# Optimization experiments

Hardware: AMD Instinct MI355X
Metric: run time of the kernel (lower is better)

The kernel has to match this reference:

```python
import jax, jax.numpy as jnp
import numpy as np

L, D_IN, D_HID, D_OUT, N = 8, 256, 1024, 256, 32768


def setup_inputs() -> dict:
    key = jax.random.key(0)
    kx, kp, kw1, kw2 = jax.random.split(key, 4)
    x = jax.random.normal(kx, (N, D_IN), dtype=jnp.float32)
    plane_idx = jax.random.randint(kp, (N,), 0, L, dtype=jnp.int32)
    W1 = jax.random.normal(kw1, (L, D_HID, D_IN), dtype=jnp.float32) * 0.014
    b1 = jnp.zeros((L, D_HID), dtype=jnp.float32)
    W2 = jax.random.normal(kw2, (L, D_OUT, D_HID), dtype=jnp.float32) * np.float32((2.0 / D_HID) ** 0.5)
    b2 = jnp.zeros((L, D_OUT), dtype=jnp.float32)
    return {"x": x, "W1": W1, "b1": b1, "W2": W2, "b2": b2, "plane_idx": plane_idx}


def reference(x, W1, b1, W2, b2, plane_idx):
    # Dense-dispatch MoE reference: scan over the L planes, run the full
    # 2-layer MLP for each plane's weights, and select per-walker rows via
    # the plane mask (equivalent math to gather -> MLP -> scatter).
    n_planes = W1.shape[0]
    out0 = jnp.zeros((x.shape[0], W2.shape[1]), dtype=x.dtype)

    def plane_step(out, p):
        h = jax.nn.gelu(x @ W1[p].T + b1[p], approximate=False)  # [N, D_hid]
        o = h @ W2[p].T + b2[p]                                  # [N, D_out]
        out = jnp.where((plane_idx == p)[:, None], o, out)
        return out, None

    out, _ = jax.lax.scan(plane_step, out0, jnp.arange(n_planes))
    return out
```

## Files before the change

kernel.cpp:

```cpp
#include <hip/hip_runtime.h>
#include <hip/hip_fp16.h>
#include <cstdint>

#define NT      32768
#define DIN     256
#define DHID    1024
#define DOUT    256
#define NPLANES 8
#define NBLK    (NT / 256)

typedef unsigned short u16;
typedef __attribute__((ext_vector_type(8))) _Float16 f16x8;
typedef __attribute__((ext_vector_type(4))) float    f32x4;

#define WS_OFFSETS 0
#define WS_META    64
#define WS_TP      1024
#define WS_TM      (WS_TP + 544*4)
#define WS_BLKHIST (WS_TM + 544*4)
#define WS_BLKBASE (WS_BLKHIST + NBLK*8*4)
#define WS_PERM    (WS_BLKBASE + NBLK*8*4)
#define WS_XB      (WS_PERM + NT*4)
#define WS_W1B     (WS_XB + NT*DIN*2)
#define WS_W2B     (WS_W1B + NPLANES*DHID*DIN*2)
#define WS_HB      (WS_W2B + NPLANES*DOUT*DHID*2)

__device__ __forceinline__ u16 f2h_bits(float f) {
    __half h = __float2half(f);
    return *reinterpret_cast<u16*>(&h);
}

__device__ __forceinline__ void gl_lds16(const void* g, void* l) {
    __builtin_amdgcn_global_load_lds(
        (const __attribute__((address_space(1))) void*)g,
        (__attribute__((address_space(3))) void*)l,
        16, 0, 0);
}

__device__ __forceinline__ float gelu_fast(float x) {
    const float u = x * (1.5957691216f + 0.07135481283f * x * x);
    const float e = __expf(-u);
    return x * __builtin_amdgcn_rcpf(1.0f + e);
}

__global__ void prep_k(const int* __restrict__ pidx, const float* __restrict__ x,
                       const float* __restrict__ W1, const float* __restrict__ W2,
                       int* __restrict__ blkhist, u16* __restrict__ xb,
                       u16* __restrict__ w1b, u16* __restrict__ w2b) {
    __shared__ int cnt[NPLANES];
    const int t = threadIdx.x, lane = t & 63;
    if ((int)blockIdx.x < NBLK) {
        if (t < NPLANES) cnt[t] = 0;
        __syncthreads();
        const int p = pidx[blockIdx.x * 256 + t];
#pragma unroll
        for (int q = 0; q < NPLANES; ++q) {
            unsigned long long m = __ballot(p == q);
            if (p == q && __popcll(m & ((1ULL << lane) - 1)) == 0)
                atomicAdd(&cnt[q], __popcll(m));
        }
        __syncthreads();
        if (t < NPLANES) blkhist[blockIdx.x * NPLANES + t] = cnt[t];
    }
    const int n0 = NT * DIN / 4, n1 = NPLANES * DHID * DIN / 4, n2 = NPLANES * DOUT * DHID / 4;
    const int stride = gridDim.x * blockDim.x;
    for (int i = blockIdx.x * blockDim.x + t; i < n0 + n1 + n2; i += stride) {
        const float4* s; ushort4* d; int j;
        if (i < n0)           { s = (const float4*)x;  d = (ushort4*)xb;  j = i; }
        else if (i < n0 + n1) { s = (const float4*)W1; d = (ushort4*)w1b; j = i - n0; }
        else                  { s = (const float4*)W2; d = (ushort4*)w2b; j = i - n0 - n1; }
        float4 v = s[j];
        ushort4 o;
        o.x = f2h_bits(v.x); o.y = f2h_bits(v.y);
        o.z = f2h_bits(v.z); o.w = f2h_bits(v.w);
        d[j] = o;
    }
}

__global__ void scan_k(const int* __restrict__ blkhist, int* __restrict__ offsets,
                       int* __restrict__ blkbase, int* __restrict__ meta,
                       int* __restrict__ tp, int* __restrict__ tm) {
    __shared__ int tot[NPLANES];
    const int t = threadIdx.x;
    if (t < NPLANES) {
        int s = 0;
#pragma unroll 8
        for (int b = 0; b < NBLK; ++b) s += blkhist[b * NPLANES + t];
        tot[t] = s;
    }
    __syncthreads();
    if (t == 0) {
        int off = 0, tc = 0;
        for (int p = 0; p < NPLANES; ++p) {
            offsets[p] = off;
            for (int m = 0; m < tot[p]; m += 64) { tp[tc] = p; tm[tc] = m; ++tc; }
            off += tot[p];
        }
        offsets[NPLANES] = off;
        meta[0] = tc;
    }
    __syncthreads();
    if (t < NPLANES) {
        int run = offsets[t];
#pragma unroll 8
        for (int b = 0; b < NBLK; ++b) {
            blkbase[b * NPLANES + t] = run;
            run += blkhist[b * NPLANES + t];
        }
    }
}

__global__ void scatter_k(const int* __restrict__ pidx, const int* __restrict__ blkbase,
                          int* __restrict__ perm) {
    __shared__ int wcnt[4][NPLANES];
    __shared__ int wbase[4][NPLANES];
    const int t = threadIdx.x, lane = t & 63, wave = t >> 6;
    const int i = blockIdx.x * 256 + t;
    const int p = pidx[i];
    int rank = 0;
#pragma unroll
    for (int q = 0; q < NPLANES; ++q) {
        unsigned long long m = __ballot(p == q);
        if (lane == 0) wcnt[wave][q] = __popcll(m);
        if (p == q) rank = __popcll(m & ((1ULL << lane) - 1));
    }
    __syncthreads();
    if (t < NPLANES) {
        int run = blkbase[blockIdx.x * NPLANES + t];
#pragma unroll
        for (int w = 0; w < 4; ++w) { wbase[w][t] = run; run += wcnt[w][t]; }
    }
    __syncthreads();
    perm[wbase[wave][p] + rank] = i;
}

#define XCD_MAP(NSPLIT)                                                        \
    const int ntiles = meta[0];                                                \
    const int xcd = blockIdx.x & 7, idx = blockIdx.x >> 3;                     \
    const int q8 = ntiles >> 3, r8 = ntiles & 7;                               \
    const int tn = q8 + (xcd < r8 ? 1 : 0);                                    \
    if (idx >= tn * (NSPLIT)) return;                                          \
    const int tile = (xcd < r8 ? xcd * (q8 + 1)                                \
                               : r8 * (q8 + 1) + (xcd - r8) * q8)              \
                     + idx / (NSPLIT);                                         \
    const int n0v = (idx % (NSPLIT)) * 128;

__global__ __launch_bounds__(256, 6) void gemm1_k(
    const u16* __restrict__ xb, const u16* __restrict__ w1b,
    const float* __restrict__ b1, const int* __restrict__ perm,
    const int* __restrict__ offsets, const int* __restrict__ meta,
    const int* __restrict__ tp, const int* __restrict__ tm,
    u16* __restrict__ hb)
{
    __shared__ __align__(16) u16 smem[12288];
    XCD_MAP(8)
    const int p   = tp[tile];
    const int m0  = tm[tile];
    const int off = offsets[p];
    const int cnt = offsets[p + 1] - off;

    u16* const sA = smem;
    u16* const sB = smem + 4096;

    const int tid = threadIdx.x;
    const u16* aptr[2];
    const u16* bptr[4];
#pragma unroll
    for (int c = 0; c < 2; ++c) {
        const int slot = c * 256 + tid, row = slot >> 3, ch = slot & 7;
        const int gr = min(m0 + row, cnt - 1);
        aptr[c] = xb + (size_t)perm[off + gr] * DIN + ((ch ^ (row & 7)) * 8);
    }
#pragma unroll
    for (int c = 0; c < 4; ++c) {
        const int slot = c * 256 + tid, row = slot >> 3, ch = slot & 7;
        bptr[c] = w1b + ((size_t)p * DHID + n0v + row) * DIN + ((ch ^ (row & 7)) * 8);
    }
    const int wave = tid >> 6, lane = tid & 63;
    const int wr = wave >> 1, wc = wave & 1;
    const int lm = lane & 15, lk = lane >> 4;

    f32x4 acc[2][4];
#pragma unroll
    for (int a = 0; a < 2; ++a)
#pragma unroll
        for (int b = 0; b < 4; ++b) acc[a][b] = (f32x4){0.f, 0.f, 0.f, 0.f};

    for (int kt = 0; kt < DIN / 64; ++kt) {
        const int k0 = kt * 64;
#pragma unroll
        for (int c = 0; c < 2; ++c) gl_lds16(aptr[c] + k0, sA + c * 2048 + tid * 8);
#pragma unroll
        for (int c = 0; c < 4; ++c) gl_lds16(bptr[c] + k0, sB + c * 2048 + tid * 8);
        __syncthreads();
#pragma unroll
        for (int kk = 0; kk < 2; ++kk) {
            f16x8 af[2], bf[4];
#pragma unroll
            for (int mf = 0; mf < 2; ++mf) {
                const int row = wr * 32 + mf * 16 + lm;
                const int g   = kk * 4 + lk;
                af[mf] = *(const f16x8*)(sA + row * 64 + ((g ^ (row & 7)) * 8));
            }
#pragma unroll
            for (int nf = 0; nf < 4; ++nf) {
                const int row = wc * 64 + nf * 16 + lm;
                const int g   = kk * 4 + lk;
                bf[nf] = *(const f16x8*)(sB + row * 64 + ((g ^ (row & 7)) * 8));
            }
#pragma unroll
            for (int mf = 0; mf < 2; ++mf)
#pragma unroll
                for (int nf = 0; nf < 4; ++nf)
                    acc[mf][nf] = __builtin_amdgcn_mfma_f32_16x16x32_f16(
                        af[mf], bf[nf], acc[mf][nf], 0, 0, 0);
        }
        __syncthreads();
    }

    u16* const sOut = smem;
#pragma unroll
    for (int nf = 0; nf < 4; ++nf) {
        const int col = wc * 64 + nf * 16 + lm;
        const float bb = b1[p * DHID + n0v + col];
        const int cc = col >> 3, c7 = col & 7;
#pragma unroll
        for (int mf = 0; mf < 2; ++mf) {
#pragma unroll
            for (int j = 0; j < 4; ++j) {
                const int tok = wr * 32 + mf * 16 + lk * 4 + j;
                sOut[tok * 128 + ((cc ^ (tok & 15)) * 8) + c7] =
                    f2h_bits(gelu_fast(acc[mf][nf][j] + bb));
            }
        }
    }
    __syncthreads();
    const int r = tid >> 2, qq = tid & 3;
    if (m0 + r < cnt) {
        u16* dst = hb + (size_t)(off + m0 + r) * DHID + n0v;
#pragma unroll
        for (int c = 0; c < 4; ++c) {
            const int l = qq * 4 + c;
            *(int4*)(dst + l * 8) = *(const int4*)(sOut + r * 128 + ((l ^ (r & 15)) * 8));
        }
    }
}

__global__ __launch_bounds__(256, 3) void gemm2_k(
    const u16* __restrict__ hb, const u16* __restrict__ w2b,
    const float* __restrict__ b2, const int* __restrict__ perm,
    const int* __restrict__ offsets, const int* __restrict__ meta,
    const int* __restrict__ tp, const int* __restrict__ tm,
    float* __restrict__ out)
{
    __shared__ __align__(16) u16 smem[24576];
    XCD_MAP(2)
    const int p   = tp[tile];
    const int m0  = tm[tile];
    const int off = offsets[p];
    const int cnt = offsets[p + 1] - off;

    u16* const sA = smem;
    u16* const sB = smem + 8192;

    const int tid = threadIdx.x;
    const u16* aptr[4];
#pragma unroll
    for (int c = 0; c < 4; ++c) {
        const int slot = c * 256 + tid, row = slot >> 4, ch = slot & 15;
        aptr[c] = hb + (size_t)(off + min(m0 + row, cnt - 1)) * DHID + ((ch ^ (row & 15)) * 8);
    }
    const u16* bptr[8];
#pragma unroll
    for (int c = 0; c < 8; ++c) {
        const int slot = c * 256 + tid, row = slot >> 4, ch = slot & 15;
        bptr[c] = w2b + ((size_t)p * DOUT + n0v + row) * DHID + ((ch ^ (row & 15)) * 8);
    }
    const int wave = tid >> 6, lane = tid & 63;
    const int wr = wave >> 1, wc = wave & 1;
    const int lm = lane & 15, lk = lane >> 4;

    f32x4 acc[2][4];
#pragma unroll
    for (int a = 0; a < 2; ++a)
#pragma unroll
        for (int b = 0; b < 4; ++b) acc[a][b] = (f32x4){0.f, 0.f, 0.f, 0.f};

    for (int kt = 0; kt < DHID / 128; ++kt) {
        const int k0 = kt * 128;
#pragma unroll
        for (int c = 0; c < 4; ++c) gl_lds16(aptr[c] + k0, sA + c * 2048 + tid * 8);
#pragma unroll
        for (int c = 0; c < 8; ++c) gl_lds16(bptr[c] + k0, sB + c * 2048 + tid * 8);
        __syncthreads();
#pragma unroll
        for (int kk = 0; kk < 4; ++kk) {
            f16x8 af[2], bf[4];
#pragma unroll
            for (int mf = 0; mf < 2; ++mf) {
                const int row = wr * 32 + mf * 16 + lm;
                const int g   = kk * 4 + lk;
                af[mf] = *(const f16x8*)(sA + row * 128 + ((g ^ (row & 15)) * 8));
            }
#pragma unroll
            for (int nf = 0; nf < 4; ++nf) {
                const int row = wc * 64 + nf * 16 + lm;
                const int g   = kk * 4 + lk;
                bf[nf] = *(const f16x8*)(sB + row * 128 + ((g ^ (row & 15)) * 8));
            }
#pragma unroll
            for (int mf = 0; mf < 2; ++mf)
#pragma unroll
                for (int nf = 0; nf < 4; ++nf)
                    acc[mf][nf] = __builtin_amdgcn_mfma_f32_16x16x32_f16(
                        af[mf], bf[nf], acc[mf][nf], 0, 0, 0);
        }
        __syncthreads();
    }

#pragma unroll
    for (int nf = 0; nf < 4; ++nf) {
        const int col = n0v + wc * 64 + nf * 16 + lm;
        const float bb = b2[p * DOUT + col];
#pragma unroll
        for (int mf = 0; mf < 2; ++mf) {
#pragma unroll
            for (int j = 0; j < 4; ++j) {
                const int tok = wr * 32 + mf * 16 + lk * 4 + j;
                if (m0 + tok < cnt)
                    out[(size_t)perm[off + m0 + tok] * DOUT + col] = acc[mf][nf][j] + bb;
            }
        }
    }
}

extern "C" void kernel_launch(void* const* d_in, const int* in_sizes, int n_in,
                              void* d_out, int out_size, void* d_ws, size_t ws_size,
                              hipStream_t stream) {
    const float* x    = (const float*)d_in[0];
    const float* W1   = (const float*)d_in[1];
    const float* b1   = (const float*)d_in[2];
    const float* W2   = (const float*)d_in[3];
    const float* b2   = (const float*)d_in[4];
    const int*   pidx = (const int*)d_in[5];
    float*       out  = (float*)d_out;

    char* ws      = (char*)d_ws;
    int* offsets  = (int*)(ws + WS_OFFSETS);
    int* meta     = (int*)(ws + WS_META);
    int* tp       = (int*)(ws + WS_TP);
    int* tm       = (int*)(ws + WS_TM);
    int* blkhist  = (int*)(ws + WS_BLKHIST);
    int* blkbase  = (int*)(ws + WS_BLKBASE);
    int* perm     = (int*)(ws + WS_PERM);
    u16* xb       = (u16*)(ws + WS_XB);
    u16* w1b      = (u16*)(ws + WS_W1B);
    u16* w2b      = (u16*)(ws + WS_W2B);
    u16* hb       = (u16*)(ws + WS_HB);

    prep_k<<<2048, 256, 0, stream>>>(pidx, x, W1, W2, blkhist, xb, w1b, w2b);
    scan_k<<<1, 64, 0, stream>>>(blkhist, offsets, blkbase, meta, tp, tm);
    scatter_k<<<NBLK, 256, 0, stream>>>(pidx, blkbase, perm);

    gemm1_k<<<4224, 256, 0, stream>>>(xb, w1b, b1, perm, offsets, meta, tp, tm, hb);
    gemm2_k<<<1056, 256, 0, stream>>>(hb, w2b, b2, perm, offsets, meta, tp, tm, out);
}
```

Measured before the change: 114.7 us.

## Unify GEMM kernels with double-buffered LDS weights and direct-to-register A loads

```diff
diff --git a/kernel.cpp b/kernel.cpp
--- a/kernel.cpp
+++ b/kernel.cpp
@@ -145,190 +145,149 @@
                      + idx / (NSPLIT);                                         \
     const int n0v = (idx % (NSPLIT)) * 128;
 
-__global__ __launch_bounds__(256, 6) void gemm1_k(
-    const u16* __restrict__ xb, const u16* __restrict__ w1b,
-    const float* __restrict__ b1, const int* __restrict__ perm,
+#define LOADA(dst, KTX)                                                        \
+    {                                                                          \
+        _Pragma("unroll") for (int mf = 0; mf < 2; ++mf) {                     \
+            const u16* ar = mf ? arow1 : arow0;                                \
+            _Pragma("unroll") for (int ks = 0; ks < 2; ++ks)                   \
+                dst[mf][ks] = *(const f16x8*)(ar + (KTX) * 64 + ks * 32);      \
+        }                                                                      \
+    }
+#define STAGEW(buf, KTX)                                                       \
+    {                                                                          \
+        _Pragma("unroll") for (int c = 0; c < 4; ++c)                          \
+            gl_lds16(wsrc[c] + (KTX) * 64, (buf) + c * 2048 + tid * 8);        \
+    }
+#define COMPUTE(buf, a)                                                        \
+    {                                                                          \
+        _Pragma("unroll") for (int kk = 0; kk < 2; ++kk) {                     \
+            f16x8 bf[4];                                                       \
+            _Pragma("unroll") for (int nf = 0; nf < 4; ++nf) {                 \
+                const int row = wc * 64 + nf * 16 + lm;                        \
+                bf[nf] = *(const f16x8*)((buf) + row * 64 +                    \
+                                         (((kk * 4 + lk) ^ (row & 7)) * 8));   \
+            }                                                                  \
+            _Pragma("unroll") for (int mf = 0; mf < 2; ++mf)                   \
+                _Pragma("unroll") for (int nf = 0; nf < 4; ++nf)               \
+                    acc[mf][nf] = __builtin_amdgcn_mfma_f32_16x16x32_f16(      \
+                        a[mf][kk], bf[nf], acc[mf][nf], 0, 0, 0);              \
+        }                                                                      \
+    }
+
+template<bool L1>
+__global__ __launch_bounds__(256, 4) void gemm_k(
+    const u16* __restrict__ A, const u16* __restrict__ W,
+    const float* __restrict__ bias, const int* __restrict__ perm,
     const int* __restrict__ offsets, const int* __restrict__ meta,
     const int* __restrict__ tp, const int* __restrict__ tm,
-    u16* __restrict__ hb)
+    void* __restrict__ Out)
 {
-    __shared__ __align__(16) u16 smem[12288];
-    XCD_MAP(8)
+    constexpr int K      = L1 ? DIN : DHID;
+    constexpr int ND     = L1 ? DHID : DOUT;
+    constexpr int KT     = K / 64;
+    constexpr int NSPLIT = ND / 128;
+
+    __shared__ __align__(16) u16 smem[16384];
+    XCD_MAP(NSPLIT)
     const int p   = tp[tile];
     const int m0  = tm[tile];
     const int off = offsets[p];
     const int cnt = offsets[p + 1] - off;
 
-    u16* const sA = smem;
-    u16* const sB = smem + 4096;
-
     const int tid = threadIdx.x;
-    const u16* aptr[2];
-    const u16* bptr[4];
-#pragma unroll
-    for (int c = 0; c < 2; ++c) {
-        const int slot = c * 256 + tid, row = slot >> 3, ch = slot & 7;
-        const int gr = min(m0 + row, cnt - 1);
-        aptr[c] = xb + (size_t)perm[off + gr] * DIN + ((ch ^ (row & 7)) * 8);
-    }
-#pragma unroll
-    for (int c = 0; c < 4; ++c) {
-        const int slot = c * 256 + tid, row = slot >> 3, ch = slot & 7;
-        bptr[c] = w1b + ((size_t)p * DHID + n0v + row) * DIN + ((ch ^ (row & 7)) * 8);
-    }
     const int wave = tid >> 6, lane = tid & 63;
     const int wr = wave >> 1, wc = wave & 1;
     const int lm = lane & 15, lk = lane >> 4;
 
+    const u16* arow0;
+    const u16* arow1;
+    {
+        const int r0 = min(m0 + wr * 32 + lm,      cnt - 1);
+        const int r1 = min(m0 + wr * 32 + 16 + lm, cnt - 1);
+        if (L1) {
+            arow0 = A + (size_t)perm[off + r0] * K;
+            arow1 = A + (size_t)perm[off + r1] * K;
+        } else {
+            arow0 = A + (size_t)(off + r0) * K;
+            arow1 = A + (size_t)(off + r1) * K;
+        }
+        arow0 += lk * 8;
+        arow1 += lk * 8;
+    }
+    const u16* wsrc[4];
+#pragma unroll
+    for (int c = 0; c < 4; ++c) {
+        const int slot = c * 256 + tid, row = slot >> 3, ch = slot & 7;
+        wsrc[c] = W + ((size_t)p * ND + n0v + row) * K + ((ch ^ (row & 7)) * 8);
+    }
+    u16* const buf0 = smem;
+    u16* const buf1 = smem + 8192;
+
     f32x4 acc[2][4];
 #pragma unroll
     for (int a = 0; a < 2; ++a)
 #pragma unroll
         for (int b = 0; b < 4; ++b) acc[a][b] = (f32x4){0.f, 0.f, 0.f, 0.f};
 
-    for (int kt = 0; kt < DIN / 64; ++kt) {
-        const int k0 = kt * 64;
-#pragma unroll
-        for (int c = 0; c < 2; ++c) gl_lds16(aptr[c] + k0, sA + c * 2048 + tid * 8);
-#pragma unroll
-        for (int c = 0; c < 4; ++c) gl_lds16(bptr[c] + k0, sB + c * 2048 + tid * 8);
+    f16x8 aC[2][2], aN[2][2];
+
+    LOADA(aC, 0)
+    STAGEW(buf0, 0)
+    __syncthreads();
+
+#pragma unroll
+    for (int kt = 0; kt < KT; kt += 2) {
+        if (kt + 1 < KT) { LOADA(aN, kt + 1) STAGEW(buf1, kt + 1) }
+        COMPUTE(buf0, aC)
         __syncthreads();
-#pragma unroll
-        for (int kk = 0; kk < 2; ++kk) {
-            f16x8 af[2], bf[4];
+        if (kt + 1 < KT) {
+            if (kt + 2 < KT) { LOADA(aC, kt + 2) STAGEW(buf0, kt + 2) }
+            COMPUTE(buf1, aN)
+            __syncthreads();
+        }
+    }
+
+    if (L1) {
+        u16* const sOut = smem;
+#pragma unroll
+        for (int nf = 0; nf < 4; ++nf) {
+            const int col = wc * 64 + nf * 16 + lm;
+            const float bb = bias[p * ND + n0v + col];
+            const int cc = col >> 3, c7 = col & 7;
 #pragma unroll
             for (int mf = 0; mf < 2; ++mf) {
-                const int row = wr * 32 + mf * 16 + lm;
-                const int g   = kk * 4 + lk;
-                af[mf] = *(const f16x8*)(sA + row * 64 + ((g ^ (row & 7)) * 8));
+#pragma unroll
+                for (int j = 0; j < 4; ++j) {
+                    const int tok = wr * 32 + mf * 16 + lk * 4 + j;
+                    sOut[tok * 128 + ((cc ^ (tok & 15)) * 8) + c7] =
+                        f2h_bits(gelu_fast(acc[mf][nf][j] + bb));
+                }
             }
-#pragma unroll
-            for (int nf = 0; nf < 4; ++nf) {
-                const int row = wc * 64 + nf * 16 + lm;
-                const int g   = kk * 4 + lk;
-                bf[nf] = *(const f16x8*)(sB + row * 64 + ((g ^ (row & 7)) * 8));
+        }
+        __syncthreads();
+        const int r = tid >> 2, qq = tid & 3;
+        if (m0 + r < cnt) {
+            u16* dst = (u16*)Out + (size_t)(off + m0 + r) * DHID + n0v;
+#pragma unroll
+            for (int c = 0; c < 4; ++c) {
+                const int l = qq * 4 + c;
+                *(int4*)(dst + l * 8) = *(const int4*)(sOut + r * 128 + ((l ^ (r & 15)) * 8));
             }
-#pragma unroll
-            for (int mf = 0; mf < 2; ++mf)
-#pragma unroll
-                for (int nf = 0; nf < 4; ++nf)
-                    acc[mf][nf] = __builtin_amdgcn_mfma_f32_16x16x32_f16(
-                        af[mf], bf[nf], acc[mf][nf], 0, 0, 0);
-        }
-        __syncthreads();
-    }
-
-    u16* const sOut = smem;
-#pragma unroll
-    for (int nf = 0; nf < 4; ++nf) {
-        const int col = wc * 64 + nf * 16 + lm;
-        const float bb = b1[p * DHID + n0v + col];
-        const int cc = col >> 3, c7 = col & 7;
-#pragma unroll
-        for (int mf = 0; mf < 2; ++mf) {
-#pragma unroll
-            for (int j = 0; j < 4; ++j) {
-                const int tok = wr * 32 + mf * 16 + lk * 4 + j;
-                sOut[tok * 128 + ((cc ^ (tok & 15)) * 8) + c7] =
-                    f2h_bits(gelu_fast(acc[mf][nf][j] + bb));
-            }
-        }
-    }
-    __syncthreads();
-    const int r = tid >> 2, qq = tid & 3;
-    if (m0 + r < cnt) {
-        u16* dst = hb + (size_t)(off + m0 + r) * DHID + n0v;
-#pragma unroll
-        for (int c = 0; c < 4; ++c) {
-            const int l = qq * 4 + c;
-            *(int4*)(dst + l * 8) = *(const int4*)(sOut + r * 128 + ((l ^ (r & 15)) * 8));
-        }
-    }
-}
-
-__global__ __launch_bounds__(256, 3) void gemm2_k(
-    const u16* __restrict__ hb, const u16* __restrict__ w2b,
-    const float* __restrict__ b2, const int* __restrict__ perm,
-    const int* __restrict__ offsets, const int* __restrict__ meta,
-    const int* __restrict__ tp, const int* __restrict__ tm,
-    float* __restrict__ out)
-{
-    __shared__ __align__(16) u16 smem[24576];
-    XCD_MAP(2)
-    const int p   = tp[tile];
-    const int m0  = tm[tile];
-    const int off = offsets[p];
-    const int cnt = offsets[p + 1] - off;
-
-    u16* const sA = smem;
-    u16* const sB = smem + 8192;
-
-    const int tid = threadIdx.x;
-    const u16* aptr[4];
-#pragma unroll
-    for (int c = 0; c < 4; ++c) {
-        const int slot = c * 256 + tid, row = slot >> 4, ch = slot & 15;
-        aptr[c] = hb + (size_t)(off + min(m0 + row, cnt - 1)) * DHID + ((ch ^ (row & 15)) * 8);
-    }
-    const u16* bptr[8];
-#pragma unroll
-    for (int c = 0; c < 8; ++c) {
-        const int slot = c * 256 + tid, row = slot >> 4, ch = slot & 15;
-        bptr[c] = w2b + ((size_t)p * DOUT + n0v + row) * DHID + ((ch ^ (row & 15)) * 8);
-    }
-    const int wave = tid >> 6, lane = tid & 63;
-    const int wr = wave >> 1, wc = wave & 1;
-    const int lm = lane & 15, lk = lane >> 4;
-
-    f32x4 acc[2][4];
-#pragma unroll
-    for (int a = 0; a < 2; ++a)
-#pragma unroll
-        for (int b = 0; b < 4; ++b) acc[a][b] = (f32x4){0.f, 0.f, 0.f, 0.f};
-
-    for (int kt = 0; kt < DHID / 128; ++kt) {
-        const int k0 = kt * 128;
-#pragma unroll
-        for (int c = 0; c < 4; ++c) gl_lds16(aptr[c] + k0, sA + c * 2048 + tid * 8);
-#pragma unroll
-        for (int c = 0; c < 8; ++c) gl_lds16(bptr[c] + k0, sB + c * 2048 + tid * 8);
-        __syncthreads();
-#pragma unroll
-        for (int kk = 0; kk < 4; ++kk) {
-            f16x8 af[2], bf[4];
+        }
+    } else {
+#pragma unroll
+        for (int nf = 0; nf < 4; ++nf) {
+            const int col = n0v + wc * 64 + nf * 16 + lm;
+            const float bb = bias[p * ND + col];
 #pragma unroll
             for (int mf = 0; mf < 2; ++mf) {
-                const int row = wr * 32 + mf * 16 + lm;
-                const int g   = kk * 4 + lk;
-                af[mf] = *(const f16x8*)(sA + row * 128 + ((g ^ (row & 15)) * 8));
-            }
-#pragma unroll
-            for (int nf = 0; nf < 4; ++nf) {
-                const int row = wc * 64 + nf * 16 + lm;
-                const int g   = kk * 4 + lk;
-                bf[nf] = *(const f16x8*)(sB + row * 128 + ((g ^ (row & 15)) * 8));
-            }
-#pragma unroll
-            for (int mf = 0; mf < 2; ++mf)
-#pragma unroll
-                for (int nf = 0; nf < 4; ++nf)
-                    acc[mf][nf] = __builtin_amdgcn_mfma_f32_16x16x32_f16(
-                        af[mf], bf[nf], acc[mf][nf], 0, 0, 0);
-        }
-        __syncthreads();
-    }
-
-#pragma unroll
-    for (int nf = 0; nf < 4; ++nf) {
-        const int col = n0v + wc * 64 + nf * 16 + lm;
-        const float bb = b2[p * DOUT + col];
-#pragma unroll
-        for (int mf = 0; mf < 2; ++mf) {
-#pragma unroll
-            for (int j = 0; j < 4; ++j) {
-                const int tok = wr * 32 + mf * 16 + lk * 4 + j;
-                if (m0 + tok < cnt)
-                    out[(size_t)perm[off + m0 + tok] * DOUT + col] = acc[mf][nf][j] + bb;
+#pragma unroll
+                for (int j = 0; j < 4; ++j) {
+                    const int tok = wr * 32 + mf * 16 + lk * 4 + j;
+                    if (m0 + tok < cnt)
+                        ((float*)Out)[(size_t)perm[off + m0 + tok] * DOUT + col] =
+                            acc[mf][nf][j] + bb;
+                }
             }
         }
     }
@@ -362,6 +321,8 @@
     scan_k<<<1, 64, 0, stream>>>(blkhist, offsets, blkbase, meta, tp, tm);
     scatter_k<<<NBLK, 256, 0, stream>>>(pidx, blkbase, perm);
 
-    gemm1_k<<<4224, 256, 0, stream>>>(xb, w1b, b1, perm, offsets, meta, tp, tm, hb);
-    gemm2_k<<<1056, 256, 0, stream>>>(hb, w2b, b2, perm, offsets, meta, tp, tm, out);
-}
+    gemm_k<true ><<<4224, 256, 0, stream>>>(xb, w1b, b1, perm, offsets, meta,
+                                            tp, tm, (void*)hb);
+    gemm_k<false><<<1056, 256, 0, stream>>>(hb, w2b, b2, perm, offsets, meta,
+                                            tp, tm, (void*)out);
+}
```

New measurement: 153.7 us. 34.0% more time.

## Make gemm1 persistent with the weight slice resident in LDS and double-buffered A

Applied to the files above, without the earlier changes.

```diff
diff --git a/kernel.cpp b/kernel.cpp
--- a/kernel.cpp
+++ b/kernel.cpp
@@ -134,6 +134,123 @@
     perm[wbase[wave][p] + rank] = i;
 }
 
+__global__ __launch_bounds__(256, 2) void gemm1_k(
+    const u16* __restrict__ xb, const u16* __restrict__ w1b,
+    const float* __restrict__ b1, const int* __restrict__ perm,
+    const int* __restrict__ offsets, u16* __restrict__ hb)
+{
+    extern __shared__ __align__(16) u16 smem[];
+    u16* const sB  = smem;
+    u16* const sA0 = smem + 32768;
+    u16* const sA1 = smem + 36864;
+
+    const int p     = blockIdx.x & 7;
+    const int chunk = (blockIdx.x >> 3) & 7;
+    const int mg    = blockIdx.x >> 6;
+    const int off = offsets[p];
+    const int cnt = offsets[p + 1] - off;
+    if (cnt <= 0) return;
+    const int nt  = (cnt + 63) >> 6;
+    const int n0v = chunk * 128;
+
+    const int tid = threadIdx.x;
+    const int wave = tid >> 6, lane = tid & 63;
+    const int wr = wave >> 1, wc = wave & 1;
+    const int lm = lane & 15, lk = lane >> 4;
+
+    {
+        const u16* wbase = w1b + ((size_t)p * DHID + n0v) * DIN;
+#pragma unroll
+        for (int c = 0; c < 16; ++c) {
+            const int slot = c * 256 + tid;
+            const int row = slot >> 5, ch = slot & 31;
+            gl_lds16(wbase + row * DIN + ((ch ^ (row & 31)) * 8), sB + slot * 8);
+        }
+    }
+
+    const int ar0 = tid >> 3,        ac0 = tid & 7;
+    const int ar1 = (256 + tid) >> 3, ac1 = (256 + tid) & 7;
+
+#define STAGE_A(buf, a0p, a1p, kt) do {                                        \
+        gl_lds16((a0p) + (kt) * 64, (buf) + tid * 8);                          \
+        gl_lds16((a1p) + (kt) * 64, (buf) + 2048 + tid * 8); } while (0)
+
+#define COMPUTE1(buf, kt) do {                                                 \
+        _Pragma("unroll") for (int kk = 0; kk < 2; ++kk) {                     \
+            const int g = kk * 4 + lk;                                         \
+            f16x8 af[2], bf[4];                                                \
+            _Pragma("unroll") for (int mf = 0; mf < 2; ++mf) {                 \
+                const int r = wr * 32 + mf * 16 + lm;                          \
+                af[mf] = *(const f16x8*)((buf) + r * 64 + ((g ^ (r & 7)) * 8));\
+            }                                                                  \
+            _Pragma("unroll") for (int nf = 0; nf < 4; ++nf) {                 \
+                const int r = wc * 64 + nf * 16 + lm;                          \
+                const int cci = (kt) * 8 + g;                                  \
+                bf[nf] = *(const f16x8*)(sB + r * 256 + ((cci ^ (r & 31)) * 8));\
+            }                                                                  \
+            _Pragma("unroll") for (int mf = 0; mf < 2; ++mf)                   \
+                _Pragma("unroll") for (int nf = 0; nf < 4; ++nf)               \
+                    acc[mf][nf] = __builtin_amdgcn_mfma_f32_16x16x32_f16(      \
+                        af[mf], bf[nf], acc[mf][nf], 0, 0, 0);                 \
+        } } while (0)
+
+    for (int mt = mg; mt < nt; mt += 8) {
+        const int m0 = mt * 64;
+        const u16* a0 = xb + (size_t)perm[off + min(m0 + ar0, cnt - 1)] * DIN
+                           + ((ac0 ^ (ar0 & 7)) * 8);
+        const u16* a1 = xb + (size_t)perm[off + min(m0 + ar1, cnt - 1)] * DIN
+                           + ((ac1 ^ (ar1 & 7)) * 8);
+
+        f32x4 acc[2][4];
+#pragma unroll
+        for (int a = 0; a < 2; ++a)
+#pragma unroll
+            for (int b = 0; b < 4; ++b) acc[a][b] = (f32x4){0.f, 0.f, 0.f, 0.f};
+
+        STAGE_A(sA0, a0, a1, 0);
+        __syncthreads();
+
+#pragma unroll
+        for (int kt = 0; kt < 4; ++kt) {
+            u16* const cur = (kt & 1) ? sA1 : sA0;
+            u16* const nxt = (kt & 1) ? sA0 : sA1;
+            if (kt < 3) STAGE_A(nxt, a0, a1, kt + 1);
+            COMPUTE1(cur, kt);
+            __syncthreads();
+        }
+
+        u16* const sOut = sA0;
+#pragma unroll
+        for (int nf = 0; nf < 4; ++nf) {
+            const int col = wc * 64 + nf * 16 + lm;
+            const float bb = b1[p * DHID + n0v + col];
+            const int cc = col >> 3, c7 = col & 7;
+#pragma unroll
+            for (int mf = 0; mf < 2; ++mf) {
+#pragma unroll
+                for (int j = 0; j < 4; ++j) {
+                    const int tok = wr * 32 + mf * 16 + lk * 4 + j;
+                    sOut[tok * 128 + ((cc ^ (tok & 15)) * 8) + c7] =
+                        f2h_bits(gelu_fast(acc[mf][nf][j] + bb));
+                }
+            }
+        }
+        __syncthreads();
+        const int r = tid >> 2, qq = tid & 3;
+        if (m0 + r < cnt) {
+            u16* dst = hb + (size_t)(off + m0 + r) * DHID + n0v;
+#pragma unroll
+            for (int c = 0; c < 4; ++c) {
+                const int l = qq * 4 + c;
+                *(int4*)(dst + l * 8) = *(const int4*)(sOut + r * 128 + ((l ^ (r & 15)) * 8));
+            }
+        }
+        __syncthreads();
+    }
+#undef STAGE_A
+#undef COMPUTE1
+}
+
 #define XCD_MAP(NSPLIT)                                                        \
     const int ntiles = meta[0];                                                \
     const int xcd = blockIdx.x & 7, idx = blockIdx.x >> 3;                     \
@@ -144,107 +261,6 @@
                                : r8 * (q8 + 1) + (xcd - r8) * q8)              \
                      + idx / (NSPLIT);                                         \
     const int n0v = (idx % (NSPLIT)) * 128;
-
-__global__ __launch_bounds__(256, 6) void gemm1_k(
-    const u16* __restrict__ xb, const u16* __restrict__ w1b,
-    const float* __restrict__ b1, const int* __restrict__ perm,
-    const int* __restrict__ offsets, const int* __restrict__ meta,
-    const int* __restrict__ tp, const int* __restrict__ tm,
-    u16* __restrict__ hb)
-{
-    __shared__ __align__(16) u16 smem[12288];
-    XCD_MAP(8)
-    const int p   = tp[tile];
-    const int m0  = tm[tile];
-    const int off = offsets[p];
-    const int cnt = offsets[p + 1] - off;
-
-    u16* const sA = smem;
-    u16* const sB = smem + 4096;
-
-    const int tid = threadIdx.x;
-    const u16* aptr[2];
-    const u16* bptr[4];
-#pragma unroll
-    for (int c = 0; c < 2; ++c) {
-        const int slot = c * 256 + tid, row = slot >> 3, ch = slot & 7;
-        const int gr = min(m0 + row, cnt - 1);
-        aptr[c] = xb + (size_t)perm[off + gr] * DIN + ((ch ^ (row & 7)) * 8);
-    }
-#pragma unroll
-    for (int c = 0; c < 4; ++c) {
-        const int slot = c * 256 + tid, row = slot >> 3, ch = slot & 7;
-        bptr[c] = w1b + ((size_t)p * DHID + n0v + row) * DIN + ((ch ^ (row & 7)) * 8);
-    }
-    const int wave = tid >> 6, lane = tid & 63;
-    const int wr = wave >> 1, wc = wave & 1;
-    const int lm = lane & 15, lk = lane >> 4;
-
-    f32x4 acc[2][4];
-#pragma unroll
-    for (int a = 0; a < 2; ++a)
-#pragma unroll
-        for (int b = 0; b < 4; ++b) acc[a][b] = (f32x4){0.f, 0.f, 0.f, 0.f};
-
-    for (int kt = 0; kt < DIN / 64; ++kt) {
-        const int k0 = kt * 64;
-#pragma unroll
-        for (int c = 0; c < 2; ++c) gl_lds16(aptr[c] + k0, sA + c * 2048 + tid * 8);
-#pragma unroll
-        for (int c = 0; c < 4; ++c) gl_lds16(bptr[c] + k0, sB + c * 2048 + tid * 8);
-        __syncthreads();
-#pragma unroll
-        for (int kk = 0; kk < 2; ++kk) {
-            f16x8 af[2], bf[4];
-#pragma unroll
-            for (int mf = 0; mf < 2; ++mf) {
-                const int row = wr * 32 + mf * 16 + lm;
-                const int g   = kk * 4 + lk;
-                af[mf] = *(const f16x8*)(sA + row * 64 + ((g ^ (row & 7)) * 8));
-            }
-#pragma unroll
-            for (int nf = 0; nf < 4; ++nf) {
-                const int row = wc * 64 + nf * 16 + lm;
-                const int g   = kk * 4 + lk;
-                bf[nf] = *(const f16x8*)(sB + row * 64 + ((g ^ (row & 7)) * 8));
-            }
-#pragma unroll
-            for (int mf = 0; mf < 2; ++mf)
-#pragma unroll
-                for (int nf = 0; nf < 4; ++nf)
-                    acc[mf][nf] = __builtin_amdgcn_mfma_f32_16x16x32_f16(
-                        af[mf], bf[nf], acc[mf][nf], 0, 0, 0);
-        }
-        __syncthreads();
-    }
-
-    u16* const sOut = smem;
-#pragma unroll
-    for (int nf = 0; nf < 4; ++nf) {
-        const int col = wc * 64 + nf * 16 + lm;
-        const float bb = b1[p * DHID + n0v + col];
-        const int cc = col >> 3, c7 = col & 7;
-#pragma unroll
-        for (int mf = 0; mf < 2; ++mf) {
-#pragma unroll
-            for (int j = 0; j < 4; ++j) {
-                const int tok = wr * 32 + mf * 16 + lk * 4 + j;
-                sOut[tok * 128 + ((cc ^ (tok & 15)) * 8) + c7] =
-                    f2h_bits(gelu_fast(acc[mf][nf][j] + bb));
-            }
-        }
-    }
-    __syncthreads();
-    const int r = tid >> 2, qq = tid & 3;
-    if (m0 + r < cnt) {
-        u16* dst = hb + (size_t)(off + m0 + r) * DHID + n0v;
-#pragma unroll
-        for (int c = 0; c < 4; ++c) {
-            const int l = qq * 4 + c;
-            *(int4*)(dst + l * 8) = *(const int4*)(sOut + r * 128 + ((l ^ (r & 15)) * 8));
-        }
-    }
-}
 
 __global__ __launch_bounds__(256, 3) void gemm2_k(
     const u16* __restrict__ hb, const u16* __restrict__ w2b,
@@ -358,10 +374,13 @@
     u16* w2b      = (u16*)(ws + WS_W2B);
     u16* hb       = (u16*)(ws + WS_HB);
 
+    (void)hipFuncSetAttribute((const void*)gemm1_k,
+                              hipFuncAttributeMaxDynamicSharedMemorySize, 81920);
+
     prep_k<<<2048, 256, 0, stream>>>(pidx, x, W1, W2, blkhist, xb, w1b, w2b);
     scan_k<<<1, 64, 0, stream>>>(blkhist, offsets, blkbase, meta, tp, tm);
     scatter_k<<<NBLK, 256, 0, stream>>>(pidx, blkbase, perm);
 
-    gemm1_k<<<4224, 256, 0, stream>>>(xb, w1b, b1, perm, offsets, meta, tp, tm, hb);
+    gemm1_k<<<512, 256, 81920, stream>>>(xb, w1b, b1, perm, offsets, hb);
     gemm2_k<<<1056, 256, 0, stream>>>(hb, w2b, b2, perm, offsets, meta, tp, tm, out);
 }
```

After: 120.4 us. 1.05x slower.
